# Kernel tuning notes

Hardware: AMD Instinct MI355X
Metric: run time of the kernel (lower is better)

The kernel has to match this reference:

```python
import jax, jax.numpy as jnp
import numpy as np

D_MODEL = 512
D_INNER = 1024   # expand * d_model
D_STATE = 16
D_CONV = 4
DT_RANK = 32     # ceil(d_model / 16)
BATCH = 8
SEQ = 1024


def _mamba(x, in_w, conv_w, conv_b, xp_w, dt_w, dt_b, A_log, Dp, out_w):
    # x: [B, L, d_model]
    Bb, Ls, _ = x.shape
    u, z = jnp.split(x @ in_w.T, 2, axis=-1)          # each [B, L, d_inner]
    # causal depthwise conv1d, kernel D_CONV, left-padded then truncated to L
    up = jnp.pad(u, ((0, 0), (D_CONV - 1, 0), (0, 0)))
    uc = conv_b + sum(up[:, k:k + Ls, :] * conv_w[:, k] for k in range(D_CONV))
    u = jax.nn.silu(uc)
    dbl = u @ xp_w.T                                   # [B, L, dt_rank+2*d_state]
    dt, Bm, Cm = jnp.split(dbl, [DT_RANK, DT_RANK + D_STATE], axis=-1)
    delta = jax.nn.softplus(dt @ dt_w.T + dt_b)        # [B, L, d_inner]
    A = -jnp.exp(A_log)                                # [d_inner, d_state]

    def step(h, inp):
        d_t, B_t, C_t, u_t = inp                       # [B,di],[B,ds],[B,ds],[B,di]
        h = h * jnp.exp(d_t[..., None] * A) + (d_t * u_t)[..., None] * B_t[:, None, :]
        return h, jnp.einsum('bds,bs->bd', h, C_t)

    h0 = jnp.zeros((Bb, D_INNER, D_STATE), x.dtype)
    xs = tuple(jnp.swapaxes(a, 0, 1) for a in (delta, Bm, Cm, u))
    _, ys = jax.lax.scan(step, h0, xs)                 # ys: [L, B, d_inner]
    y = jnp.swapaxes(ys, 0, 1) + u * Dp
    return (y * jax.nn.silu(z)) @ out_w.T              # [B, L, d_model]


def _params(key):
    ks = jax.random.split(key, 5)
    s = 0.02
    return {
        'in_w': jax.random.normal(ks[0], (2 * D_INNER, D_MODEL)) * s,
        'conv_w': jax.random.normal(ks[1], (D_INNER, D_CONV)) * 0.3,
        'conv_b': jnp.zeros((D_INNER,)),
        'xp_w': jax.random.normal(ks[2], (DT_RANK + 2 * D_STATE, D_INNER)) * s,
        'dt_w': jax.random.normal(ks[3], (D_INNER, DT_RANK)) * (DT_RANK ** -0.5),
        'dt_b': jnp.full((D_INNER,), -4.0),
        'A_log': jnp.log(jnp.tile(jnp.arange(1, D_STATE + 1, dtype=jnp.float32), (D_INNER, 1))),
        'D': jnp.ones((D_INNER,)),
        'out_w': jax.random.normal(ks[4], (D_MODEL, D_INNER)) * s,
    }


def setup_inputs():
    key = jax.random.key(0)
    kx, kf, kb = jax.random.split(key, 3)
    inp = {'x': jax.random.normal(kx, (BATCH, SEQ, D_MODEL), dtype=jnp.float32)}
    for n, v in _params(kf).items():
        inp[n + '_f'] = v
    for n, v in _params(kb).items():
        inp[n + '_b'] = v
    return inp


def reference(x, in_w_f, conv_w_f, conv_b_f, xp_w_f, dt_w_f, dt_b_f, A_log_f, D_f, out_w_f,
              in_w_b, conv_w_b, conv_b_b, xp_w_b, dt_w_b, dt_b_b, A_log_b, D_b, out_w_b):
    fwd = _mamba(x, in_w_f, conv_w_f, conv_b_f, xp_w_f, dt_w_f, dt_b_f, A_log_f, D_f, out_w_f)
    bwd = _mamba(x[:, ::-1, :], in_w_b, conv_w_b, conv_b_b, xp_w_b, dt_w_b, dt_b_b,
                 A_log_b, D_b, out_w_b)[:, ::-1, :]
    return fwd + bwd
```

## Files before the change

kernel.cpp:

```cpp
#include <hip/hip_runtime.h>
#include <math.h>

#define BATCH 8
#define SEQ 1024
#define D_MODEL 512
#define D_INNER 1024
#define D_STATE 16
#define DT_RANK 32
#define NROWS (BATCH * SEQ)
#define CH 64
#define CL 16
#define USLAB 8388608l

typedef short short8 __attribute__((ext_vector_type(8)));
typedef float f32x4 __attribute__((ext_vector_type(4)));

__device__ __forceinline__ float sigmoidf_(float x) { return 1.f / (1.f + __expf(-x)); }

__device__ __forceinline__ float softplus_(float v) {
  return (v > 20.f) ? v : __logf(1.f + __expf(v));
}

__device__ __forceinline__ ushort f2b(float f) {
  uint u = __float_as_uint(f);
  return (ushort)((u + 0x7FFFu + ((u >> 16) & 1u)) >> 16);
}
__device__ __forceinline__ float b2f(ushort u) {
  return __uint_as_float(((uint)u) << 16);
}

__device__ __forceinline__ void gload16(const ushort* g, const ushort* l) {
  __builtin_amdgcn_global_load_lds(
      (const __attribute__((address_space(1))) void*)g,
      (__attribute__((address_space(3))) void*)l, 16, 0, 0);
}

__device__ __forceinline__ int revrow(int m) {
  return (m & ~1023) | (1023 - (m & 1023));
}

__global__ __launch_bounds__(512, 2) void inproj256(
    const ushort* __restrict__ A, int lda,
    const ushort* __restrict__ B, int ldb,
    ushort* __restrict__ Cu, ushort* __restrict__ Cz,
    int K)
{
  __shared__ ushort As[3][256 * 32];
  __shared__ ushort Bs[3][256 * 32];
  const int tid = threadIdx.x;
  const int w = tid >> 6, lane = tid & 63;

  const int nwg = gridDim.x * gridDim.y;
  int bid = blockIdx.y * gridDim.x + blockIdx.x;
  int wgid = (bid & 7) * (nwg >> 3) + (bid >> 3);
  const int bm = (wgid / gridDim.x) * 256;
  const int bn = (wgid % gridDim.x) * 256;

  const int wr = w >> 2, wc = w & 3;
  const int rw0 = wr * 128, cw0 = wc * 64;
  const int srow = w * 16 + (lane >> 2);
  const int scol = (((lane & 3) ^ ((lane >> 3) & 3)) << 3);
  const int rchunk = (((lane >> 4) ^ (((lane & 15) >> 1) & 3)) << 3);

  f32x4 acc[8][4] = {};

  auto stageA = [&](int buf, int k0, int half) {
    int gm = bm + half * 128 + srow;
    gload16(A + (long)gm * lda + k0 + scol, &As[buf][(half * 128 + w * 16) * 32]);
  };
  auto stageB = [&](int buf, int k0, int half) {
    int gn = bn + half * 128 + srow;
    gload16(B + (long)gn * ldb + k0 + scol, &Bs[buf][(half * 128 + w * 16) * 32]);
  };

  const int NT = K >> 5;
  stageA(0, 0, 0); stageA(0, 0, 1); stageB(0, 0, 0); stageB(0, 0, 1);
  stageA(1, 32, 0); stageA(1, 32, 1); stageB(1, 32, 0); stageB(1, 32, 1);
  asm volatile("s_waitcnt vmcnt(4)" ::: "memory");
  __builtin_amdgcn_s_barrier();

  int buf = 0;
  for (int t = 0; t < NT; ++t) {
    const int kf = (t + 2) << 5;
    const int sbuf = (buf >= 1) ? buf - 1 : buf + 2;
    short8 a0[4], b0[4];
#pragma unroll
    for (int i = 0; i < 4; ++i)
      a0[i] = *(const short8*)&As[buf][(rw0 + i * 16 + (lane & 15)) * 32 + rchunk];
#pragma unroll
    for (int j = 0; j < 4; ++j)
      b0[j] = *(const short8*)&Bs[buf][(cw0 + j * 16 + (lane & 15)) * 32 + rchunk];
    if (t + 2 < NT) { stageA(sbuf, kf, 0); stageA(sbuf, kf, 1); }
    __builtin_amdgcn_s_barrier();
    __builtin_amdgcn_s_setprio(1);
#pragma unroll
    for (int i = 0; i < 4; ++i)
#pragma unroll
      for (int j = 0; j < 4; ++j)
        acc[i][j] = __builtin_amdgcn_mfma_f32_16x16x32_bf16(a0[i], b0[j], acc[i][j], 0, 0, 0);
    __builtin_amdgcn_s_setprio(0);
    __builtin_amdgcn_s_barrier();
    short8 a1[4];
#pragma unroll
    for (int i = 0; i < 4; ++i)
      a1[i] = *(const short8*)&As[buf][(rw0 + 64 + i * 16 + (lane & 15)) * 32 + rchunk];
    if (t + 2 < NT) {
      stageB(sbuf, kf, 0); stageB(sbuf, kf, 1);
      asm volatile("s_waitcnt vmcnt(4)" ::: "memory");
    } else if (t + 1 < NT) {
      asm volatile("s_waitcnt vmcnt(0)" ::: "memory");
    }
    __builtin_amdgcn_s_barrier();
    __builtin_amdgcn_s_setprio(1);
#pragma unroll
    for (int i = 0; i < 4; ++i)
#pragma unroll
      for (int j = 0; j < 4; ++j)
        acc[4 + i][j] = __builtin_amdgcn_mfma_f32_16x16x32_bf16(a1[i], b0[j], acc[4 + i][j], 0, 0, 0);
    __builtin_amdgcn_s_setprio(0);
    __builtin_amdgcn_s_barrier();
    buf = (buf == 2) ? 0 : buf + 1;
  }

  const int bdir = bn >> 11;
  const int bz = ((bn & 2047) >= 1024);
  const int bncol = bn & 1023;
  ushort* Cp = (bz ? Cz : Cu) + (long)bdir * USLAB;
  ushort* scr = &As[0][0] + w * 1024;

#pragma unroll
  for (int i = 0; i < 8; ++i) {
#pragma unroll
    for (int r = 0; r < 4; ++r)
#pragma unroll
      for (int j = 0; j < 4; ++j) {
        float v = acc[i][j][r];
        if (bz) v = v * sigmoidf_(v);
        scr[((lane >> 4) * 4 + r) * 64 + j * 16 + (lane & 15)] = f2b(v);
      }
#pragma unroll
    for (int q = 0; q < 2; ++q) {
      int r16 = (lane >> 3) + q * 8;
      short8 pk = *(const short8*)&scr[r16 * 64 + (lane & 7) * 8];
      int m = bm + rw0 + i * 16 + r16;
      int row = bdir ? revrow(m) : m;
      *(short8*)&Cp[(long)row * 1024 + bncol + cw0 + (lane & 7) * 8] = pk;
    }
  }
}

template<int BM, int BN, int RW, int CW, int EPI, int DUALK, int MDIAG>
__global__ __launch_bounds__(256) void gemm_bf16(
    const ushort* __restrict__ A, int lda, const ushort* __restrict__ A2,
    const ushort* __restrict__ B, int ldb, const ushort* __restrict__ B2,
    float* __restrict__ Cf, ushort* __restrict__ Cb, ushort* __restrict__ Cb2,
    int ldc, int K, const float* __restrict__ bias, const float* __restrict__ bias2,
    int b_stride, int revC, int accumC)
{
  constexpr int MI = BM / RW / 16;
  constexpr int NJ = BN / CW / 16;
  __shared__ ushort As[2][BM * 32];
  __shared__ ushort Bs[2][BN * 32];
  const int tid = threadIdx.x;
  const int w = tid >> 6, lane = tid & 63;

  const int nwg = gridDim.x * gridDim.y;
  int bid = blockIdx.y * gridDim.x + blockIdx.x;
  int wgid = (bid & 7) * (nwg >> 3) + (bid >> 3);
  const int bm = (wgid / gridDim.x) * BM;
  const int bn = (wgid % gridDim.x) * BN;

  if (MDIAG) {
    int mdir = (bm >= NROWS) ? 1 : 0;
    B += mdir * b_stride;
    if (mdir) bias = bias2;
  }

  const int rw0 = (w / CW) * (MI * 16);
  const int cw0 = (w % CW) * (NJ * 16);
  const int srow = w * 16 + (lane >> 2);
  const int scol = (((lane & 3) ^ ((lane >> 3) & 3)) << 3);
  const int rchunk = (((lane >> 4) ^ (((lane & 15) >> 1) & 3)) << 3);

  f32x4 acc[MI][NJ] = {};

  auto stage = [&](int buf, int k0) {
    const ushort* Ap = A;
    const ushort* Bp = B;
    int kc = k0;
    bool hi = false;
    if (DUALK && k0 >= (K >> 1)) { Ap = A2; Bp = B2; kc = k0 - (K >> 1); hi = true; }
#pragma unroll
    for (int it = 0; it < BM / 64; ++it) {
      int gm = bm + it * 64 + srow;
      int arow = (DUALK && hi) ? revrow(gm) : gm;
      gload16(Ap + (long)arow * lda + kc + scol, &As[buf][(it * 64 + w * 16) * 32]);
    }
#pragma unroll
    for (int it = 0; it < BN / 64; ++it) {
      int gn = bn + it * 64 + srow;
      gload16(Bp + (long)gn * ldb + kc + scol, &Bs[buf][(it * 64 + w * 16) * 32]);
    }
  };

  stage(0, 0);
  __syncthreads();

  for (int k0 = 0; k0 < K; k0 += 32) {
    int cur = (k0 >> 5) & 1;
    if (k0 + 32 < K) stage(cur ^ 1, k0 + 32);
    short8 a[MI], b[NJ];
#pragma unroll
    for (int i = 0; i < MI; ++i)
      a[i] = *(const short8*)&As[cur][(rw0 + i * 16 + (lane & 15)) * 32 + rchunk];
#pragma unroll
    for (int j = 0; j < NJ; ++j)
      b[j] = *(const short8*)&Bs[cur][(cw0 + j * 16 + (lane & 15)) * 32 + rchunk];
#pragma unroll
    for (int i = 0; i < MI; ++i)
#pragma unroll
      for (int j = 0; j < NJ; ++j)
        acc[i][j] = __builtin_amdgcn_mfma_f32_16x16x32_bf16(a[i], b[j], acc[i][j], 0, 0, 0);
    __syncthreads();
  }

  if (EPI == 1) {
    ushort* scr = &As[0][0] + w * 1024;
#pragma unroll
    for (int i = 0; i < MI; ++i) {
#pragma unroll
      for (int r = 0; r < 4; ++r)
#pragma unroll
        for (int j = 0; j < NJ; ++j) {
          int n = bn + cw0 + j * 16 + (lane & 15);
          float v = softplus_(acc[i][j][r] + bias[n]);
          scr[((lane >> 4) * 4 + r) * 64 + j * 16 + (lane & 15)] = f2b(v);
        }
#pragma unroll
      for (int q = 0; q < 2; ++q) {
        int r16 = (lane >> 3) + q * 8;
        short8 pk = *(const short8*)&scr[r16 * 64 + (lane & 7) * 8];
        int m = bm + rw0 + i * 16 + r16;
        *(short8*)&Cb[(long)m * ldc + bn + cw0 + (lane & 7) * 8] = pk;
      }
    }
  } else if (EPI == 0 && !revC && !accumC) {
    float* scrf = (float*)&As[0][0] + w * 1024;
#pragma unroll
    for (int i = 0; i < MI; ++i) {
#pragma unroll
      for (int r = 0; r < 4; ++r)
#pragma unroll
        for (int j = 0; j < NJ; ++j)
          scrf[((lane >> 4) * 4 + r) * 64 + j * 16 + (lane & 15)] = acc[i][j][r];
#pragma unroll
      for (int q = 0; q < 4; ++q) {
        int r16 = (lane >> 4) + q * 4;
        float4 pk = *(const float4*)&scrf[r16 * 64 + (lane & 15) * 4];
        int m = bm + rw0 + i * 16 + r16;
        *(float4*)&Cf[(long)m * ldc + bn + cw0 + (lane & 15) * 4] = pk;
      }
    }
  } else {
#pragma unroll
    for (int i = 0; i < MI; ++i)
#pragma unroll
      for (int r = 0; r < 4; ++r) {
        int m = bm + rw0 + i * 16 + (lane >> 4) * 4 + r;
        int crow = revC ? revrow(m) : m;
#pragma unroll
        for (int j = 0; j < NJ; ++j) {
          int n = bn + cw0 + j * 16 + (lane & 15);
          float v = acc[i][j][r];
          if (EPI == 0) {
            float* p = Cf + (long)crow * ldc + n;
            if (accumC) *p += v; else *p = v;
          } else {
            Cb[(long)crow * ldc + n] = f2b(v);
          }
        }
      }
  }
}

struct Seg { const float4* s; ushort4* d; int n4; int bstart; };
struct ConvArgs { Seg seg[9]; };

__global__ __launch_bounds__(256) void convert_all(ConvArgs a)
{
  int blk = blockIdx.x;
  int i = 0;
#pragma unroll
  for (int k = 1; k < 9; ++k) if (blk >= a.seg[k].bstart) i = k;
  int idx = (blk - a.seg[i].bstart) * 256 + threadIdx.x;
  if (idx >= a.seg[i].n4) return;
  float4 v = a.seg[i].s[idx];
  ushort4 o;
  o.x = f2b(v.x); o.y = f2b(v.y); o.z = f2b(v.z); o.w = f2b(v.w);
  a.seg[i].d[idx] = o;
}

__global__ __launch_bounds__(256) void conv_silu(
    const ushort* __restrict__ u_bf,
    const float* __restrict__ cw_f, const float* __restrict__ cw_b,
    const float* __restrict__ cb_f, const float* __restrict__ cb_b,
    ushort* __restrict__ uc_bf)
{
  long i = (long)blockIdx.x * 256 + threadIdx.x;
  int dir = (int)(i >> 20);
  int r = (int)(i >> 7) & 8191;
  int d0 = ((int)i & 127) << 3;
  int t = r & (SEQ - 1);
  const float* cw = dir ? cw_b : cw_f;
  const float* cb = dir ? cb_b : cb_f;
  const ushort* p = u_bf + dir * USLAB + (long)r * D_INNER + d0;
  short8 z8 = {0, 0, 0, 0, 0, 0, 0, 0};
  short8 u0 = *(const short8*)p;
  short8 u1 = (t >= 1) ? *(const short8*)(p - 1024) : z8;
  short8 u2 = (t >= 2) ? *(const short8*)(p - 2048) : z8;
  short8 u3 = (t >= 3) ? *(const short8*)(p - 3072) : z8;
  float4 bb0 = *(const float4*)(cb + d0);
  float4 bb1 = *(const float4*)(cb + d0 + 4);
  float bbv[8] = {bb0.x, bb0.y, bb0.z, bb0.w, bb1.x, bb1.y, bb1.z, bb1.w};
  short8 o;
#pragma unroll
  for (int j = 0; j < 8; ++j) {
    float4 wj = *(const float4*)(cw + (d0 + j) * 4);
    float acc = bbv[j];
    acc = fmaf(wj.w, b2f((ushort)u0[j]), acc);
    acc = fmaf(wj.z, b2f((ushort)u1[j]), acc);
    acc = fmaf(wj.y, b2f((ushort)u2[j]), acc);
    acc = fmaf(wj.x, b2f((ushort)u3[j]), acc);
    o[j] = (short)f2b(acc * sigmoidf_(acc));
  }
  *(short8*)(uc_bf + dir * USLAB + (long)r * D_INNER + d0) = o;
}

#define EP_FAST(dt, Ep)                                        \
  {                                                            \
    float E1 = __expf(-(dt));                                  \
    float E2 = E1 * E1, E4 = E2 * E2, E8 = E4 * E4;            \
    Ep[0] = E1;  Ep[1] = E2;      Ep[2] = E2 * E1;             \
    Ep[3] = E4;  Ep[4] = E4 * E1; Ep[5] = E4 * E2;             \
    Ep[6] = E4 * Ep[2]; Ep[7] = E8;  Ep[8] = E8 * E1;          \
    Ep[9] = E8 * E2; Ep[10] = E8 * Ep[2]; Ep[11] = E8 * E4;    \
    Ep[12] = E8 * Ep[4]; Ep[13] = E8 * Ep[5];                  \
    Ep[14] = E8 * Ep[6]; Ep[15] = E8 * E8;                     \
  }

__device__ __forceinline__ bool a_is_arange(const float* Ar) {
  bool ok = true;
#pragma unroll
  for (int s = 0; s < D_STATE; ++s)
    ok = ok && (fabsf(Ar[s] + (float)(s + 1)) <= 1e-3f * (float)(s + 1));
  return ok;
}

__global__ __launch_bounds__(256) void scan_partA(
    const ushort* __restrict__ delta_bf,
    const ushort* __restrict__ ucv_bf,
    const ushort* __restrict__ dblb,
    const float* __restrict__ A_log_f, const float* __restrict__ A_log_b,
    ushort* __restrict__ hend,
    float* __restrict__ dtsum_buf)
{
  __shared__ float bc[CL][16];
  long idx = (long)blockIdx.x * 256 + threadIdx.x;
  int d = (int)idx & 1023;
  int c = ((int)idx >> 10) & (CH - 1);
  int b = ((int)idx >> 16) & 7;
  int dir = (int)(idx >> 19);
  const long r0 = (long)b * SEQ + c * CL;
  const ushort* dblp = dblb + (long)dir * NROWS * 64;
  {
    int tt = threadIdx.x >> 4, ss = threadIdx.x & 15;
    bc[tt][ss] = b2f(dblp[(r0 + tt) * 64 + 32 + ss]);
  }
  const float* Alog = dir ? A_log_b : A_log_f;
  const ushort* dp = delta_bf + dir * USLAB;
  const ushort* up = ucv_bf + dir * USLAB;
  float Ar[D_STATE];
#pragma unroll
  for (int s = 0; s < D_STATE; ++s) Ar[s] = -__expf(Alog[d * D_STATE + s]);
  const bool fast = a_is_arange(Ar);
  float h[D_STATE] = {0.f};
  float dtsum = 0.f;
  __syncthreads();

  if (fast) {
    for (int t = 0; t < CL; ++t) {
      long r = r0 + t;
      float dt = b2f(dp[r * 1024 + d]);
      float u  = b2f(up[r * 1024 + d]);
      float du = dt * u;
      dtsum += dt;
      float Ep[16];
      EP_FAST(dt, Ep);
#pragma unroll
      for (int s = 0; s < D_STATE; ++s)
        h[s] = fmaf(h[s], Ep[s], du * bc[t][s]);
    }
  } else {
    for (int t = 0; t < CL; ++t) {
      long r = r0 + t;
      float dt = b2f(dp[r * 1024 + d]);
      float u  = b2f(up[r * 1024 + d]);
      float du = dt * u;
      dtsum += dt;
#pragma unroll
      for (int s = 0; s < D_STATE; ++s)
        h[s] = fmaf(h[s], __expf(dt * Ar[s]), du * bc[t][s]);
    }
  }
  long base = ((long)((dir * 8 + b) * CH + c) * D_STATE) * 1024 + d;
#pragma unroll
  for (int s = 0; s < D_STATE; ++s) hend[base + s * 1024] = f2b(h[s]);
  dtsum_buf[(long)((dir * 8 + b) * CH + c) * 1024 + d] = dtsum;
}

__global__ __launch_bounds__(256) void scan_partB(
    ushort* __restrict__ hend,
    const float* __restrict__ dtsum_buf,
    const float* __restrict__ A_log_f, const float* __restrict__ A_log_b)
{
  long idx = (long)blockIdx.x * 256 + threadIdx.x;
  int d = (int)idx & 1023;
  int s = ((int)idx >> 10) & 15;
  int b = ((int)idx >> 14) & 7;
  int dir = (int)(idx >> 17);
  const float* Alog = dir ? A_log_b : A_log_f;
  float Ars = -__expf(Alog[d * D_STATE + s]);
  float H = 0.f;
  for (int c = 0; c < CH; ++c) {
    long off = ((long)((dir * 8 + b) * CH + c) * D_STATE + s) * 1024 + d;
    float he = b2f(hend[off]);
    float P = __expf(Ars * dtsum_buf[(long)((dir * 8 + b) * CH + c) * 1024 + d]);
    hend[off] = f2b(H);
    H = fmaf(P, H, he);
  }
}

__global__ __launch_bounds__(256) void scan_partC(
    const ushort* __restrict__ delta_bf,
    const ushort* __restrict__ ucv_bf,
    const ushort* __restrict__ dblb,
    const float* __restrict__ A_log_f, const float* __restrict__ A_log_b,
    const float* __restrict__ Dp_f, const float* __restrict__ Dp_b,
    const ushort* __restrict__ zsilu_bf,
    const ushort* __restrict__ hinit,
    ushort* __restrict__ ydz_bf)
{
  __shared__ float bc[CL][32];
  long idx = (long)blockIdx.x * 256 + threadIdx.x;
  int d = (int)idx & 1023;
  int c = ((int)idx >> 10) & (CH - 1);
  int b = ((int)idx >> 16) & 7;
  int dir = (int)(idx >> 19);
  const long r0 = (long)b * SEQ + c * CL;
  const ushort* dblp = dblb + (long)dir * NROWS * 64;
  {
    int tt = threadIdx.x >> 4, cc = (threadIdx.x & 15) * 2;
    ushort2 v = *(const ushort2*)&dblp[(r0 + tt) * 64 + 32 + cc];
    bc[tt][cc] = b2f(v.x); bc[tt][cc + 1] = b2f(v.y);
  }
  const float* Alog = dir ? A_log_b : A_log_f;
  const ushort* dp = delta_bf + dir * USLAB;
  const ushort* up = ucv_bf + dir * USLAB;
  const ushort* zp = zsilu_bf + dir * USLAB;
  ushort* yp = ydz_bf + dir * USLAB;
  float Ar[D_STATE];
#pragma unroll
  for (int s = 0; s < D_STATE; ++s) Ar[s] = -__expf(Alog[d * D_STATE + s]);
  const bool fast = a_is_arange(Ar);
  float h[D_STATE];
  long base = ((long)((dir * 8 + b) * CH + c) * D_STATE) * 1024 + d;
#pragma unroll
  for (int s = 0; s < D_STATE; ++s) h[s] = b2f(hinit[base + s * 1024]);
  float Dd = (dir ? Dp_b : Dp_f)[d];
  __syncthreads();

  if (fast) {
    for (int t = 0; t < CL; ++t) {
      long r = r0 + t;
      float dt = b2f(dp[r * 1024 + d]);
      float u  = b2f(up[r * 1024 + d]);
      float du = dt * u;
      float Ep[16];
      EP_FAST(dt, Ep);
      float y = 0.f;
#pragma unroll
      for (int s = 0; s < D_STATE; ++s) {
        h[s] = fmaf(h[s], Ep[s], du * bc[t][s]);
        y = fmaf(h[s], bc[t][16 + s], y);
      }
      float zs = b2f(zp[r * 1024 + d]);
      float yv = fmaf(u, Dd, y);
      yp[r * 1024 + d] = f2b(yv * zs);
    }
  } else {
    for (int t = 0; t < CL; ++t) {
      long r = r0 + t;
      float dt = b2f(dp[r * 1024 + d]);
      float u  = b2f(up[r * 1024 + d]);
      float du = dt * u;
      float y = 0.f;
#pragma unroll
      for (int s = 0; s < D_STATE; ++s) {
        h[s] = fmaf(h[s], __expf(dt * Ar[s]), du * bc[t][s]);
        y = fmaf(h[s], bc[t][16 + s], y);
      }
      float zs = b2f(zp[r * 1024 + d]);
      float yv = fmaf(u, Dd, y);
      yp[r * 1024 + d] = f2b(yv * zs);
    }
  }
}

extern "C" void kernel_launch(void* const* d_in, const int* in_sizes, int n_in,
                              void* d_out, int out_size, void* d_ws, size_t ws_size,
                              hipStream_t stream)
{
  const float* x = (const float*)d_in[0];
  float* out = (float*)d_out;
  char* ws = (char*)d_ws;
  ushort* zsilu  = (ushort*)(ws);
  ushort* ucv    = (ushort*)(ws + (32ul << 20));
  ushort* u_bf   = (ushort*)(ws + (64ul << 20));
  ushort* hend   = (ushort*)(ws + (96ul << 20));
  float*  dtsum  = (float*)(ws + (128ul << 20));
  ushort* dblb   = (ushort*)(ws + (132ul << 20));
  ushort* out_wb = (ushort*)(ws + (134ul << 20));
  ushort* xbf    = hend;
  ushort* in_wb  = hend + (8ul << 19);
  ushort* xp_wb  = hend + (12ul << 19);
  ushort* dt_wb  = xp_wb + 131072;
  ushort* delta  = u_bf;
  ushort* ydz    = ucv;

  ConvArgs ca;
  int bcur = 0, si = 0;
  auto addseg = [&](const float* s, ushort* d, int nelem) {
    ca.seg[si].s = (const float4*)s; ca.seg[si].d = (ushort4*)d;
    ca.seg[si].n4 = nelem / 4; ca.seg[si].bstart = bcur;
    bcur += (nelem / 4 + 255) / 256; ++si;
  };
  addseg(x, xbf, NROWS * D_MODEL);
  addseg((const float*)d_in[1], in_wb, 2048 * 512);
  addseg((const float*)d_in[10], in_wb + 2048 * 512, 2048 * 512);
  addseg((const float*)d_in[9], out_wb, 512 * 1024);
  addseg((const float*)d_in[18], out_wb + 512 * 1024, 512 * 1024);
  addseg((const float*)d_in[4], xp_wb, 64 * 1024);
  addseg((const float*)d_in[13], xp_wb + 65536, 64 * 1024);
  addseg((const float*)d_in[5], dt_wb, 1024 * 32);
  addseg((const float*)d_in[14], dt_wb + 32768, 1024 * 32);

  dim3 blk(256);
  convert_all<<<dim3(bcur), blk, 0, stream>>>(ca);

  inproj256<<<dim3(4096 / 256, NROWS / 256), dim3(512), 0, stream>>>(
      xbf, D_MODEL, in_wb, D_MODEL, u_bf, zsilu, D_MODEL);
  conv_silu<<<dim3(2 * NROWS * D_INNER / 8 / 256), blk, 0, stream>>>(
      u_bf, (const float*)d_in[2], (const float*)d_in[11],
      (const float*)d_in[3], (const float*)d_in[12], ucv);
  gemm_bf16<64, 64, 2, 2, 4, 0, 1><<<dim3(1, 256), blk, 0, stream>>>(
      ucv, D_INNER, nullptr, xp_wb, D_INNER, nullptr,
      nullptr, dblb, nullptr, 64, D_INNER, nullptr, nullptr, 65536, 0, 0);
  gemm_bf16<128, 128, 2, 2, 1, 0, 1><<<dim3(8, 128), blk, 0, stream>>>(
      dblb, 64, nullptr, dt_wb, DT_RANK, nullptr,
      nullptr, delta, nullptr, D_INNER, DT_RANK,
      (const float*)d_in[6], (const float*)d_in[15], 32768, 0, 0);
  const float* Alf = (const float*)d_in[7];
  const float* Alb = (const float*)d_in[16];
  scan_partA<<<dim3(2 * BATCH * CH * 1024 / 256), blk, 0, stream>>>(
      delta, ucv, dblb, Alf, Alb, hend, dtsum);
  scan_partB<<<dim3(2 * BATCH * 16 * 1024 / 256), blk, 0, stream>>>(
      hend, dtsum, Alf, Alb);
  scan_partC<<<dim3(2 * BATCH * CH * 1024 / 256), blk, 0, stream>>>(
      delta, ucv, dblb, Alf, Alb,
      (const float*)d_in[8], (const float*)d_in[17], zsilu, hend, ydz);
  gemm_bf16<128, 128, 2, 2, 0, 1, 0><<<dim3(4, 64), blk, 0, stream>>>(
      ydz, D_INNER, ydz + USLAB, out_wb, D_INNER, out_wb + 512 * 1024,
      out, nullptr, nullptr, D_MODEL, 2 * D_INNER, nullptr, nullptr, 0, 0, 0);
}
```

Measured before the change: 259.8 us.

## Fuse causal conv+SiLU into x-projection GEMM and scan kernels, drop conv buffer

Removes the standalone conv_silu kernel and its materialised bf16 conv output. The x-projection GEMM now computes the depthwise conv and SiLU on the fly while staging its A tile. The scan kernels recompute the conv per timestep from raw u, using a small per-chunk buffer of the three preceding u values. This saves one full-size write and read of the activation tensor and one launch, at the cost of redundant conv arithmetic in three kernels. The GEMM output epilogue also loses its vectorised float4 store path, falling back to scalar stores.

```diff
diff --git a/kernel.cpp b/kernel.cpp
--- a/kernel.cpp
+++ b/kernel.cpp
@@ -149,11 +149,109 @@
   }
 }
 
+__global__ __launch_bounds__(256) void xproj_conv(
+    const ushort* __restrict__ u,
+    const ushort* __restrict__ xp_w,
+    const float* __restrict__ cw_f, const float* __restrict__ cw_b,
+    const float* __restrict__ cb_f, const float* __restrict__ cb_b,
+    ushort* __restrict__ dblb)
+{
+  __shared__ ushort As[2][64 * 32];
+  __shared__ ushort Bs[2][64 * 32];
+  const int tid = threadIdx.x;
+  const int w = tid >> 6, lane = tid & 63;
+  const int nwg = gridDim.x;
+  int wgid = (blockIdx.x & 7) * (nwg >> 3) + (blockIdx.x >> 3);
+  const int bm = wgid * 64;
+  const int mdir = (bm >= NROWS) ? 1 : 0;
+  const ushort* B = xp_w + mdir * 65536;
+  const float* cw = mdir ? cw_b : cw_f;
+  const float* cb = mdir ? cb_b : cb_f;
+
+  const int rw0 = (w >> 1) * 32;
+  const int cw0 = (w & 1) * 32;
+  const int srow = w * 16 + (lane >> 2);
+  const int scol = (((lane & 3) ^ ((lane >> 3) & 3)) << 3);
+  const int rchunk = (((lane >> 4) ^ (((lane & 15) >> 1) & 3)) << 3);
+
+  const int ri = tid >> 2, cg = tid & 3;
+  const int gr = bm + ri;
+  const int tt = gr & (SEQ - 1);
+  const int wchunk = (cg ^ ((ri >> 1) & 3)) * 8;
+
+  f32x4 acc[2][2] = {};
+  short8 z8 = {0, 0, 0, 0, 0, 0, 0, 0};
+  short8 ur0 = z8, ur1 = z8, ur2 = z8, ur3 = z8;
+
+  auto issueA = [&](int k0) {
+    const ushort* p = u + (long)gr * 1024 + k0 + cg * 8;
+    ur0 = *(const short8*)p;
+    ur1 = (tt >= 1) ? *(const short8*)(p - 1024) : z8;
+    ur2 = (tt >= 2) ? *(const short8*)(p - 2048) : z8;
+    ur3 = (tt >= 3) ? *(const short8*)(p - 3072) : z8;
+  };
+  auto convWrite = [&](int buf, int k0) {
+    int dc = k0 + cg * 8;
+    short8 o;
+#pragma unroll
+    for (int j = 0; j < 8; ++j) {
+      float4 wj = *(const float4*)(cw + (dc + j) * 4);
+      float a = cb[dc + j];
+      a = fmaf(wj.w, b2f((ushort)ur0[j]), a);
+      a = fmaf(wj.z, b2f((ushort)ur1[j]), a);
+      a = fmaf(wj.y, b2f((ushort)ur2[j]), a);
+      a = fmaf(wj.x, b2f((ushort)ur3[j]), a);
+      o[j] = (short)f2b(a * sigmoidf_(a));
+    }
+    *(short8*)&As[buf][ri * 32 + wchunk] = o;
+  };
+  auto stageB = [&](int buf, int k0) {
+    gload16(B + (long)srow * 1024 + k0 + scol, &Bs[buf][(w * 16) * 32]);
+  };
+
+  issueA(0);
+  stageB(0, 0);
+  convWrite(0, 0);
+  __syncthreads();
+
+  for (int k0 = 0; k0 < 1024; k0 += 32) {
+    int cur = (k0 >> 5) & 1;
+    bool more = (k0 + 32 < 1024);
+    if (more) { issueA(k0 + 32); stageB(cur ^ 1, k0 + 32); }
+    short8 a[2], b[2];
+#pragma unroll
+    for (int i = 0; i < 2; ++i)
+      a[i] = *(const short8*)&As[cur][(rw0 + i * 16 + (lane & 15)) * 32 + rchunk];
+#pragma unroll
+    for (int j = 0; j < 2; ++j)
+      b[j] = *(const short8*)&Bs[cur][(cw0 + j * 16 + (lane & 15)) * 32 + rchunk];
+#pragma unroll
+    for (int i = 0; i < 2; ++i)
+#pragma unroll
+      for (int j = 0; j < 2; ++j)
+        acc[i][j] = __builtin_amdgcn_mfma_f32_16x16x32_bf16(a[i], b[j], acc[i][j], 0, 0, 0);
+    if (more) convWrite(cur ^ 1, k0 + 32);
+    __syncthreads();
+  }
+
+#pragma unroll
+  for (int i = 0; i < 2; ++i)
+#pragma unroll
+    for (int r = 0; r < 4; ++r) {
+      int m = bm + rw0 + i * 16 + (lane >> 4) * 4 + r;
+#pragma unroll
+      for (int j = 0; j < 2; ++j) {
+        int n = cw0 + j * 16 + (lane & 15);
+        dblb[(long)m * 64 + n] = f2b(acc[i][j][r]);
+      }
+    }
+}
+
 template<int BM, int BN, int RW, int CW, int EPI, int DUALK, int MDIAG>
 __global__ __launch_bounds__(256) void gemm_bf16(
     const ushort* __restrict__ A, int lda, const ushort* __restrict__ A2,
     const ushort* __restrict__ B, int ldb, const ushort* __restrict__ B2,
-    float* __restrict__ Cf, ushort* __restrict__ Cb, ushort* __restrict__ Cb2,
+    float* __restrict__ Cf, ushort* __restrict__ Cb,
     int ldc, int K, const float* __restrict__ bias, const float* __restrict__ bias2,
     int b_stride, int revC, int accumC)
 {
@@ -244,23 +342,6 @@
         *(short8*)&Cb[(long)m * ldc + bn + cw0 + (lane & 7) * 8] = pk;
       }
     }
-  } else if (EPI == 0 && !revC && !accumC) {
-    float* scrf = (float*)&As[0][0] + w * 1024;
-#pragma unroll
-    for (int i = 0; i < MI; ++i) {
-#pragma unroll
-      for (int r = 0; r < 4; ++r)
-#pragma unroll
-        for (int j = 0; j < NJ; ++j)
-          scrf[((lane >> 4) * 4 + r) * 64 + j * 16 + (lane & 15)] = acc[i][j][r];
-#pragma unroll
-      for (int q = 0; q < 4; ++q) {
-        int r16 = (lane >> 4) + q * 4;
-        float4 pk = *(const float4*)&scrf[r16 * 64 + (lane & 15) * 4];
-        int m = bm + rw0 + i * 16 + r16;
-        *(float4*)&Cf[(long)m * ldc + bn + cw0 + (lane & 15) * 4] = pk;
-      }
-    }
   } else {
 #pragma unroll
     for (int i = 0; i < MI; ++i)
@@ -272,12 +353,8 @@
         for (int j = 0; j < NJ; ++j) {
           int n = bn + cw0 + j * 16 + (lane & 15);
           float v = acc[i][j][r];
-          if (EPI == 0) {
-            float* p = Cf + (long)crow * ldc + n;
-            if (accumC) *p += v; else *p = v;
-          } else {
-            Cb[(long)crow * ldc + n] = f2b(v);
-          }
+          float* p = Cf + (long)crow * ldc + n;
+          if (accumC) *p += v; else *p = v;
         }
       }
   }
@@ -298,42 +375,6 @@
   ushort4 o;
   o.x = f2b(v.x); o.y = f2b(v.y); o.z = f2b(v.z); o.w = f2b(v.w);
   a.seg[i].d[idx] = o;
-}
-
-__global__ __launch_bounds__(256) void conv_silu(
-    const ushort* __restrict__ u_bf,
-    const float* __restrict__ cw_f, const float* __restrict__ cw_b,
-    const float* __restrict__ cb_f, const float* __restrict__ cb_b,
-    ushort* __restrict__ uc_bf)
-{
-  long i = (long)blockIdx.x * 256 + threadIdx.x;
-  int dir = (int)(i >> 20);
-  int r = (int)(i >> 7) & 8191;
-  int d0 = ((int)i & 127) << 3;
-  int t = r & (SEQ - 1);
-  const float* cw = dir ? cw_b : cw_f;
-  const float* cb = dir ? cb_b : cb_f;
-  const ushort* p = u_bf + dir * USLAB + (long)r * D_INNER + d0;
-  short8 z8 = {0, 0, 0, 0, 0, 0, 0, 0};
-  short8 u0 = *(const short8*)p;
-  short8 u1 = (t >= 1) ? *(const short8*)(p - 1024) : z8;
-  short8 u2 = (t >= 2) ? *(const short8*)(p - 2048) : z8;
-  short8 u3 = (t >= 3) ? *(const short8*)(p - 3072) : z8;
-  float4 bb0 = *(const float4*)(cb + d0);
-  float4 bb1 = *(const float4*)(cb + d0 + 4);
-  float bbv[8] = {bb0.x, bb0.y, bb0.z, bb0.w, bb1.x, bb1.y, bb1.z, bb1.w};
-  short8 o;
-#pragma unroll
-  for (int j = 0; j < 8; ++j) {
-    float4 wj = *(const float4*)(cw + (d0 + j) * 4);
-    float acc = bbv[j];
-    acc = fmaf(wj.w, b2f((ushort)u0[j]), acc);
-    acc = fmaf(wj.z, b2f((ushort)u1[j]), acc);
-    acc = fmaf(wj.y, b2f((ushort)u2[j]), acc);
-    acc = fmaf(wj.x, b2f((ushort)u3[j]), acc);
-    o[j] = (short)f2b(acc * sigmoidf_(acc));
-  }
-  *(short8*)(uc_bf + dir * USLAB + (long)r * D_INNER + d0) = o;
 }
 
 #define EP_FAST(dt, Ep)                                        \
@@ -358,11 +399,14 @@
 
 __global__ __launch_bounds__(256) void scan_partA(
     const ushort* __restrict__ delta_bf,
-    const ushort* __restrict__ ucv_bf,
+    const ushort* __restrict__ u_bf,
     const ushort* __restrict__ dblb,
     const float* __restrict__ A_log_f, const float* __restrict__ A_log_b,
+    const float* __restrict__ cw_f, const float* __restrict__ cw_b,
+    const float* __restrict__ cb_f, const float* __restrict__ cb_b,
     ushort* __restrict__ hend,
-    float* __restrict__ dtsum_buf)
+    float* __restrict__ dtsum_buf,
+    ushort* __restrict__ prim)
 {
   __shared__ float bc[CL][16];
   long idx = (long)blockIdx.x * 256 + threadIdx.x;
@@ -378,35 +422,46 @@
   }
   const float* Alog = dir ? A_log_b : A_log_f;
   const ushort* dp = delta_bf + dir * USLAB;
-  const ushort* up = ucv_bf + dir * USLAB;
+  const ushort* up = u_bf + dir * USLAB;
+  const float4 wj = *(const float4*)((dir ? cw_b : cw_f) + d * 4);
+  const float cbd = (dir ? cb_b : cb_f)[d];
   float Ar[D_STATE];
 #pragma unroll
   for (int s = 0; s < D_STATE; ++s) Ar[s] = -__expf(Alog[d * D_STATE + s]);
   const bool fast = a_is_arange(Ar);
   float h[D_STATE] = {0.f};
   float dtsum = 0.f;
+  int t0 = c * CL;
+  float um1 = 0.f, um2 = 0.f, um3 = 0.f;
+  if (t0 >= 1) um1 = b2f(up[(r0 - 1) * 1024 + d]);
+  if (t0 >= 2) um2 = b2f(up[(r0 - 2) * 1024 + d]);
+  if (t0 >= 3) um3 = b2f(up[(r0 - 3) * 1024 + d]);
+  long gix = (long)((dir * 8 + b) * CH + c) * 3;
+  prim[(gix + 0) * 1024 + d] = f2b(um1);
+  prim[(gix + 1) * 1024 + d] = f2b(um2);
+  prim[(gix + 2) * 1024 + d] = f2b(um3);
   __syncthreads();
 
-  if (fast) {
-    for (int t = 0; t < CL; ++t) {
-      long r = r0 + t;
-      float dt = b2f(dp[r * 1024 + d]);
-      float u  = b2f(up[r * 1024 + d]);
-      float du = dt * u;
-      dtsum += dt;
+  for (int t = 0; t < CL; ++t) {
+    long r = r0 + t;
+    float dt = b2f(dp[r * 1024 + d]);
+    float ucur = b2f(up[r * 1024 + d]);
+    float ca = cbd;
+    ca = fmaf(wj.w, ucur, ca);
+    ca = fmaf(wj.z, um1, ca);
+    ca = fmaf(wj.y, um2, ca);
+    ca = fmaf(wj.x, um3, ca);
+    float uc = ca * sigmoidf_(ca);
+    um3 = um2; um2 = um1; um1 = ucur;
+    float du = dt * uc;
+    dtsum += dt;
+    if (fast) {
       float Ep[16];
       EP_FAST(dt, Ep);
 #pragma unroll
       for (int s = 0; s < D_STATE; ++s)
         h[s] = fmaf(h[s], Ep[s], du * bc[t][s]);
-    }
-  } else {
-    for (int t = 0; t < CL; ++t) {
-      long r = r0 + t;
-      float dt = b2f(dp[r * 1024 + d]);
-      float u  = b2f(up[r * 1024 + d]);
-      float du = dt * u;
-      dtsum += dt;
+    } else {
 #pragma unroll
       for (int s = 0; s < D_STATE; ++s)
         h[s] = fmaf(h[s], __expf(dt * Ar[s]), du * bc[t][s]);
@@ -442,13 +497,16 @@
 
 __global__ __launch_bounds__(256) void scan_partC(
     const ushort* __restrict__ delta_bf,
-    const ushort* __restrict__ ucv_bf,
+    const ushort* u_bf,
     const ushort* __restrict__ dblb,
     const float* __restrict__ A_log_f, const float* __restrict__ A_log_b,
     const float* __restrict__ Dp_f, const float* __restrict__ Dp_b,
+    const float* __restrict__ cw_f, const float* __restrict__ cw_b,
+    const float* __restrict__ cb_f, const float* __restrict__ cb_b,
     const ushort* __restrict__ zsilu_bf,
     const ushort* __restrict__ hinit,
-    ushort* __restrict__ ydz_bf)
+    const ushort* __restrict__ prim,
+    ushort* ydz_bf)
 {
   __shared__ float bc[CL][32];
   long idx = (long)blockIdx.x * 256 + threadIdx.x;
@@ -465,9 +523,11 @@
   }
   const float* Alog = dir ? A_log_b : A_log_f;
   const ushort* dp = delta_bf + dir * USLAB;
-  const ushort* up = ucv_bf + dir * USLAB;
+  const ushort* up = u_bf + dir * USLAB;
   const ushort* zp = zsilu_bf + dir * USLAB;
   ushort* yp = ydz_bf + dir * USLAB;
+  const float4 wj = *(const float4*)((dir ? cw_b : cw_f) + d * 4);
+  const float cbd = (dir ? cb_b : cb_f)[d];
   float Ar[D_STATE];
 #pragma unroll
   for (int s = 0; s < D_STATE; ++s) Ar[s] = -__expf(Alog[d * D_STATE + s]);
@@ -477,42 +537,43 @@
 #pragma unroll
   for (int s = 0; s < D_STATE; ++s) h[s] = b2f(hinit[base + s * 1024]);
   float Dd = (dir ? Dp_b : Dp_f)[d];
+  long gix = (long)((dir * 8 + b) * CH + c) * 3;
+  float um1 = b2f(prim[(gix + 0) * 1024 + d]);
+  float um2 = b2f(prim[(gix + 1) * 1024 + d]);
+  float um3 = b2f(prim[(gix + 2) * 1024 + d]);
   __syncthreads();
 
-  if (fast) {
-    for (int t = 0; t < CL; ++t) {
-      long r = r0 + t;
-      float dt = b2f(dp[r * 1024 + d]);
-      float u  = b2f(up[r * 1024 + d]);
-      float du = dt * u;
+  for (int t = 0; t < CL; ++t) {
+    long r = r0 + t;
+    float dt = b2f(dp[r * 1024 + d]);
+    float ucur = b2f(up[r * 1024 + d]);
+    float ca = cbd;
+    ca = fmaf(wj.w, ucur, ca);
+    ca = fmaf(wj.z, um1, ca);
+    ca = fmaf(wj.y, um2, ca);
+    ca = fmaf(wj.x, um3, ca);
+    float uc = ca * sigmoidf_(ca);
+    um3 = um2; um2 = um1; um1 = ucur;
+    float du = dt * uc;
+    float y = 0.f;
+    if (fast) {
       float Ep[16];
       EP_FAST(dt, Ep);
-      float y = 0.f;
 #pragma unroll
       for (int s = 0; s < D_STATE; ++s) {
         h[s] = fmaf(h[s], Ep[s], du * bc[t][s]);
         y = fmaf(h[s], bc[t][16 + s], y);
       }
-      float zs = b2f(zp[r * 1024 + d]);
-      float yv = fmaf(u, Dd, y);
-      yp[r * 1024 + d] = f2b(yv * zs);
-    }
-  } else {
-    for (int t = 0; t < CL; ++t) {
-      long r = r0 + t;
-      float dt = b2f(dp[r * 1024 + d]);
-      float u  = b2f(up[r * 1024 + d]);
-      float du = dt * u;
-      float y = 0.f;
+    } else {
 #pragma unroll
       for (int s = 0; s < D_STATE; ++s) {
         h[s] = fmaf(h[s], __expf(dt * Ar[s]), du * bc[t][s]);
         y = fmaf(h[s], bc[t][16 + s], y);
       }
-      float zs = b2f(zp[r * 1024 + d]);
-      float yv = fmaf(u, Dd, y);
-      yp[r * 1024 + d] = f2b(yv * zs);
-    }
+    }
+    float zs = b2f(zp[r * 1024 + d]);
+    float yv = fmaf(uc, Dd, y);
+    yp[r * 1024 + d] = f2b(yv * zs);
   }
 }
 
@@ -524,18 +585,18 @@
   float* out = (float*)d_out;
   char* ws = (char*)d_ws;
   ushort* zsilu  = (ushort*)(ws);
-  ushort* ucv    = (ushort*)(ws + (32ul << 20));
-  ushort* u_bf   = (ushort*)(ws + (64ul << 20));
+  ushort* u_bf   = (ushort*)(ws + (32ul << 20));
+  ushort* delta  = (ushort*)(ws + (64ul << 20));
   ushort* hend   = (ushort*)(ws + (96ul << 20));
   float*  dtsum  = (float*)(ws + (128ul << 20));
   ushort* dblb   = (ushort*)(ws + (132ul << 20));
   ushort* out_wb = (ushort*)(ws + (134ul << 20));
+  ushort* prim   = (ushort*)(ws + (136ul << 20));
   ushort* xbf    = hend;
   ushort* in_wb  = hend + (8ul << 19);
   ushort* xp_wb  = hend + (12ul << 19);
   ushort* dt_wb  = xp_wb + 131072;
-  ushort* delta  = u_bf;
-  ushort* ydz    = ucv;
+  ushort* ydz    = u_bf;
 
   ConvArgs ca;
   int bcur = 0, si = 0;
@@ -557,28 +618,30 @@
   dim3 blk(256);
   convert_all<<<dim3(bcur), blk, 0, stream>>>(ca);
 
+  const float* cwf = (const float*)d_in[2];
+  const float* cwb = (const float*)d_in[11];
+  const float* cbf = (const float*)d_in[3];
+  const float* cbb = (const float*)d_in[12];
+  const float* Alf = (const float*)d_in[7];
+  const float* Alb = (const float*)d_in[16];
+
   inproj256<<<dim3(4096 / 256, NROWS / 256), dim3(512), 0, stream>>>(
       xbf, D_MODEL, in_wb, D_MODEL, u_bf, zsilu, D_MODEL);
-  conv_silu<<<dim3(2 * NROWS * D_INNER / 8 / 256), blk, 0, stream>>>(
-      u_bf, (const float*)d_in[2], (const float*)d_in[11],
-      (const float*)d_in[3], (const float*)d_in[12], ucv);
-  gemm_bf16<64, 64, 2, 2, 4, 0, 1><<<dim3(1, 256), blk, 0, stream>>>(
-      ucv, D_INNER, nullptr, xp_wb, D_INNER, nullptr,
-      nullptr, dblb, nullptr, 64, D_INNER, nullptr, nullptr, 65536, 0, 0);
+  xproj_conv<<<dim3(256), blk, 0, stream>>>(
+      u_bf, xp_wb, cwf, cwb, cbf, cbb, dblb);
   gemm_bf16<128, 128, 2, 2, 1, 0, 1><<<dim3(8, 128), blk, 0, stream>>>(
       dblb, 64, nullptr, dt_wb, DT_RANK, nullptr,
-      nullptr, delta, nullptr, D_INNER, DT_RANK,
+      nullptr, delta, D_INNER, DT_RANK,
       (const float*)d_in[6], (const float*)d_in[15], 32768, 0, 0);
-  const float* Alf = (const float*)d_in[7];
-  const float* Alb = (const float*)d_in[16];
   scan_partA<<<dim3(2 * BATCH * CH * 1024 / 256), blk, 0, stream>>>(
-      delta, ucv, dblb, Alf, Alb, hend, dtsum);
+      delta, u_bf, dblb, Alf, Alb, cwf, cwb, cbf, cbb, hend, dtsum, prim);
   scan_partB<<<dim3(2 * BATCH * 16 * 1024 / 256), blk, 0, stream>>>(
       hend, dtsum, Alf, Alb);
   scan_partC<<<dim3(2 * BATCH * CH * 1024 / 256), blk, 0, stream>>>(
-      delta, ucv, dblb, Alf, Alb,
-      (const float*)d_in[8], (const float*)d_in[17], zsilu, hend, ydz);
+      delta, u_bf, dblb, Alf, Alb,
+      (const float*)d_in[8], (const float*)d_in[17],
+      cwf, cwb, cbf, cbb, zsilu, hend, prim, ydz);
   gemm_bf16<128, 128, 2, 2, 0, 1, 0><<<dim3(4, 64), blk, 0, stream>>>(
       ydz, D_INNER, ydz + USLAB, out_wb, D_INNER, out_wb + 512 * 1024,
-      out, nullptr, nullptr, D_MODEL, 2 * D_INNER, nullptr, nullptr, 0, 0, 0);
-}
+      out, nullptr, D_MODEL, 2 * D_INNER, nullptr, nullptr, 0, 0, 0);
+}
```

Result: slower. 307.7 us (+18.4%).
